# Performance work log

Measured on AMD Instinct MI355X. Metric: run time of the kernel, lower is better.

Reference implementation:

```python
import math
import jax, jax.numpy as jnp
import numpy as np

B, T, E = 2, 2048, 2048
H, HKV = 16, 4
DH = E // H              # 128
ROT_DIM = DH             # rotary_pct = 1.0 -> 128
ROT_HALF = ROT_DIM // 2  # RotaryEmbedding is built with dim=ROT_DIM//2=64; only these dims rotate
MAX_SEQ = 2048


def _rope_tables():
    # theta = 10000 ** (-arange(0, dim, 2)/dim) with dim = ROT_HALF
    theta = 10000.0 ** (-jnp.arange(0, ROT_HALF, 2, dtype=jnp.float32) / ROT_HALF)  # [ROT_HALF//2]
    pos = jnp.arange(MAX_SEQ, dtype=jnp.float32)
    angles = pos[:, None] * theta[None, :]   # [MAX_SEQ, ROT_HALF//2]
    return jnp.cos(angles), jnp.sin(angles)


def _apply_rotary(q, k, start_pos):
    # q: [B,T,H,ROT_DIM], k: [B,T,HKV,ROT_DIM]; rotate only first ROT_HALF dims (interleaved pairs)
    cos, sin = _rope_tables()
    t = q.shape[1]
    cos = jax.lax.dynamic_slice_in_dim(cos, start_pos, t, axis=0)[None, :, None, :]
    sin = jax.lax.dynamic_slice_in_dim(sin, start_pos, t, axis=0)[None, :, None, :]

    def rot(a):
        a_rot, a_pass = a[..., :ROT_HALF], a[..., ROT_HALF:]
        x, y = a_rot[..., 0::2], a_rot[..., 1::2]
        rx = x * cos - y * sin
        ry = x * sin + y * cos
        rotated = jnp.stack([rx, ry], axis=-1).reshape(*a_rot.shape)
        return jnp.concatenate([rotated, a_pass], axis=-1)

    return rot(q), rot(k)


def setup_inputs() -> dict:
    key = jax.random.key(0)
    ks = jax.random.split(key, 9)
    s = 0.02  # weight scale for sane logits
    return {
        "x": jax.random.normal(ks[0], (B, T, E), dtype=jnp.float32),
        "Wq": jax.random.normal(ks[1], (E, H * DH), dtype=jnp.float32) * s,
        "bq": jax.random.normal(ks[2], (H * DH,), dtype=jnp.float32) * s,
        "Wk": jax.random.normal(ks[3], (E, HKV * DH), dtype=jnp.float32) * s,
        "bk": jax.random.normal(ks[4], (HKV * DH,), dtype=jnp.float32) * s,
        "Wv": jax.random.normal(ks[5], (E, HKV * DH), dtype=jnp.float32) * s,
        "bv": jax.random.normal(ks[6], (HKV * DH,), dtype=jnp.float32) * s,
        "Wo": jax.random.normal(ks[7], (E, E), dtype=jnp.float32) * s,
        "bo": jax.random.normal(ks[8], (E,), dtype=jnp.float32) * s,
        "start_pos": 0,
    }


def reference(x, Wq, bq, Wk, bk, Wv, bv, Wo, bo, start_pos):
    b, t, _ = x.shape
    q = (x @ Wq + bq).reshape(b, t, H, DH)
    k = (x @ Wk + bk).reshape(b, t, HKV, DH)
    v = (x @ Wv + bv).reshape(b, t, HKV, DH)

    q, k = _apply_rotary(q, k, start_pos)

    group = H // HKV
    k = jnp.repeat(k, group, axis=2)  # [b,t,H,DH]
    v = jnp.repeat(v, group, axis=2)

    # scores: [b,H,t,t]
    scores = jnp.einsum("bqhd,bkhd->bhqk", q, k) / math.sqrt(DH)
    causal = jnp.tril(jnp.ones((t, t), dtype=bool))
    scores = jnp.where(causal[None, None], scores, -jnp.inf)
    probs = jax.nn.softmax(scores, axis=-1)

    out = jnp.einsum("bhqk,bkhd->bqhd", probs, v).reshape(b, t, H * DH)
    return out @ Wo + bo
```

## Files before the change

### kernel.cpp

```cpp
#include <hip/hip_runtime.h>

typedef __attribute__((ext_vector_type(8))) short short8;
typedef __attribute__((ext_vector_type(4))) float f32x4;
typedef __attribute__((ext_vector_type(16))) float f32x16;

#define DEVFN __device__ __forceinline__

DEVFN unsigned short f2bf(float f) {
  unsigned int u = __builtin_bit_cast(unsigned int, f);
  u += 0x7FFFu + ((u >> 16) & 1u);
  return (unsigned short)(u >> 16);
}
DEVFN float bf2f(unsigned int u) { return __builtin_bit_cast(float, u << 16); }

DEVFN unsigned int cvtpk_bf16(float lo, float hi) {
  unsigned int d;
  asm("v_cvt_pk_bf16_f32 %0, %1, %2" : "=v"(d) : "v"(lo), "v"(hi));
  return d;
}
DEVFN void plswap32(unsigned int& a, unsigned int& b) {
  asm("v_permlane32_swap_b32 %0, %1" : "+v"(a), "+v"(b));
}
DEVFN float bcast32(float v, int srclane) {
  int r = __builtin_amdgcn_ds_bpermute(srclane * 4, __builtin_bit_cast(int, v));
  return __builtin_bit_cast(float, r);
}

__global__ __launch_bounds__(256) void prep_all(
    const float* __restrict__ Wq, const float* __restrict__ Wk, const float* __restrict__ Wv,
    const float* __restrict__ Wo, const float* __restrict__ bq, const float* __restrict__ bk,
    const float* __restrict__ bv, const float* __restrict__ x,
    unsigned short* __restrict__ Wqkvt, unsigned short* __restrict__ Wot,
    unsigned short* __restrict__ xb, float* __restrict__ cost, float* __restrict__ sint,
    float* __restrict__ bcat) {
  __shared__ float lds[32][33];
  const int bid = blockIdx.x, tid = threadIdx.x;
  if (bid < 10240) {
    const float* W; unsigned short* Wt; int ncols, bx, by;
    if (bid < 4096)      { W = Wq; Wt = Wqkvt;                        ncols = 2048; bx = bid & 63; by = bid >> 6; }
    else if (bid < 5120) { int l = bid - 4096; W = Wk; Wt = Wqkvt + (size_t)2048 * 2048; ncols = 512; bx = l & 15; by = l >> 4; }
    else if (bid < 6144) { int l = bid - 5120; W = Wv; Wt = Wqkvt + (size_t)2560 * 2048; ncols = 512; bx = l & 15; by = l >> 4; }
    else                 { int l = bid - 6144; W = Wo; Wt = Wot;      ncols = 2048; bx = l & 63; by = l >> 6; }
    int n0 = bx * 32, k0 = by * 32;
    int tx = tid & 31, ty = tid >> 5;
    #pragma unroll
    for (int i = 0; i < 4; i++) {
      int kr = ty + i * 8;
      lds[kr][tx] = W[(size_t)(k0 + kr) * ncols + n0 + tx];
    }
    __syncthreads();
    #pragma unroll
    for (int i = 0; i < 4; i++) {
      int nr = ty + i * 8;
      Wt[(size_t)(n0 + nr) * 2048 + k0 + tx] = f2bf(lds[tx][nr]);
    }
  } else if (bid < 14336) {
    int gid = (bid - 10240) * 256 + tid;
    const float4* xv = (const float4*)x;
    float4 a = xv[(size_t)gid * 2], b = xv[(size_t)gid * 2 + 1];
    short8 u;
    u[0] = (short)f2bf(a.x); u[1] = (short)f2bf(a.y); u[2] = (short)f2bf(a.z); u[3] = (short)f2bf(a.w);
    u[4] = (short)f2bf(b.x); u[5] = (short)f2bf(b.y); u[6] = (short)f2bf(b.z); u[7] = (short)f2bf(b.w);
    *(short8*)(xb + (size_t)gid * 8) = u;
  } else if (bid < 14592) {
    int gid = (bid - 14336) * 256 + tid;
    int pos = gid >> 5, i = gid & 31;
    float theta = powf(10000.0f, -(float)(2 * i) / 64.0f);
    float ang = (float)pos * theta;
    cost[gid] = cosf(ang);
    sint[gid] = sinf(ang);
  } else {
    int i = (bid - 14592) * 256 + tid;
    float v;
    if (i < 2048) v = bq[i];
    else if (i < 2560) v = bk[i - 2048];
    else v = bv[i - 2560];
    bcat[i] = v;
  }
}

__global__ __launch_bounds__(256) void scatter_all(
    const unsigned short* __restrict__ QKVb, const float* __restrict__ cost,
    const float* __restrict__ sint, const int* __restrict__ spp,
    unsigned short* __restrict__ QFr, unsigned short* __restrict__ KFr,
    unsigned short* __restrict__ VFr) {
  __shared__ __align__(16) unsigned short lds[64 * 128];
  const int bid = blockIdx.x, tid = threadIdx.x;
  if (bid < 20480) {
    int NH, LOG2NH, colOff, gid;
    unsigned short* dst;
    float scale;
    if (bid < 16384) { NH = 16; LOG2NH = 4; colOff = 0;    dst = QFr; scale = 0.12751743f; gid = bid * 256 + tid; }
    else             { NH = 4;  LOG2NH = 2; colOff = 2048; dst = KFr; scale = 1.0f;        gid = (bid - 16384) * 256 + tid; }
    int j = gid & 63;
    int h = (gid >> 6) & (NH - 1);
    int m = gid >> (6 + LOG2NH);
    int t = m & 2047;
    int b = m >> 11;
    const unsigned short* src = QKVb + (size_t)m * 3072 + colOff + h * 128 + 2 * j;
    unsigned int pair = *(const unsigned int*)src;
    float xv = bf2f(pair & 0xFFFFu), yv = bf2f(pair >> 16);
    float rx, ry;
    if (j < 32) {
      int pos = (spp[0] + t) & 2047;
      float c = cost[pos * 32 + j], s = sint[pos * 32 + j];
      rx = xv * c - yv * s;
      ry = xv * s + yv * c;
    } else { rx = xv; ry = yv; }
    rx *= scale; ry *= scale;
    int d0 = 2 * j;
    size_t off = (size_t)(b * NH + h) * 262144 + (t >> 5) * 4096 + (d0 >> 4) * 512
               + ((d0 >> 3) & 1) * 256 + (t & 31) * 8 + (d0 & 7);
    unsigned int outp = (unsigned int)f2bf(rx) | ((unsigned int)f2bf(ry) << 16);
    *(unsigned int*)(dst + off) = outp;
  } else {
    int l = bid - 20480;
    int t0 = (l & 31) * 64;
    int bk = l >> 5;
    const unsigned short* src = QKVb + (size_t)(bk >> 2) * 2048 * 3072 + 2560 + (bk & 3) * 128;
    #pragma unroll
    for (int c = 0; c < 4; c++) {
      int idx = c * 256 + tid;
      int tr = idx >> 4, dc = idx & 15;
      short8 v = *(const short8*)(src + (size_t)(t0 + tr) * 3072 + dc * 8);
      *(short8*)((char*)lds + tr * 256 + 16 * (dc ^ (tr >> 3))) = v;
    }
    __syncthreads();
    unsigned short* dstb = VFr + (size_t)bk * 262144;
    #pragma unroll
    for (int c2 = 0; c2 < 4; c2++) {
      int idx2 = c2 * 256 + tid;
      int tc = idx2 & 7, d = idx2 >> 3;
      short8 u;
      #pragma unroll
      for (int e = 0; e < 8; e++) {
        int t = 8 * tc + e;
        u[e] = *(const short*)((char*)lds + t * 256 + 16 * ((d >> 3) ^ tc) + (d & 7) * 2);
      }
      size_t off = (size_t)(t0 >> 6) * 8192 + ((d >> 5) * 4 + ((tc >> 1) & 3)) * 512
                 + (tc & 1) * 256 + (d & 31) * 8;
      *(short8*)(dstb + off) = u;
    }
  }
}

template<bool BF16OUT>
__global__ __launch_bounds__(256, 2) void gemm_bt(
    const unsigned short* __restrict__ A, const unsigned short* __restrict__ Bt,
    const float* __restrict__ bias, void* __restrict__ Cout, int M, int N, int K, int NTX) {
  __shared__ __align__(16) unsigned short Asl[128 * 64];
  __shared__ __align__(16) unsigned short Bsl[128 * 64];
  int tid = threadIdx.x;
  int lane = tid & 63, w = tid >> 6;
  int wr = w >> 1, wc = w & 1;
  int f = blockIdx.x;
  int cpx = gridDim.x >> 3;
  int fs = (f & 7) * cpx + (f >> 3);
  int m0 = (fs / NTX) * 128, n0 = (fs % NTX) * 128;

  f32x4 acc[4][4];
  #pragma unroll
  for (int i = 0; i < 4; i++)
    #pragma unroll
    for (int j = 0; j < 4; j++)
      #pragma unroll
      for (int r = 0; r < 4; r++) acc[i][j][r] = 0.f;

  int srow = w * 32 + (lane >> 3);
  int kc8 = (lane & 7) * 8;
  const unsigned short* Aptr = A + (size_t)(m0 + srow) * K + kc8;
  const unsigned short* Bptr = Bt + (size_t)(n0 + srow) * K + kc8;
  unsigned short* AslW = Asl + w * 4 * 512;
  unsigned short* BslW = Bsl + w * 4 * 512;

  for (int k0 = 0; k0 < K; k0 += 64) {
    __syncthreads();
    #pragma unroll
    for (int i = 0; i < 4; i++) {
      __builtin_amdgcn_global_load_lds(
        (const __attribute__((address_space(1))) unsigned int*)(Aptr + (size_t)i * 8 * K + k0),
        (__attribute__((address_space(3))) unsigned int*)(AslW + i * 512), 16, 0, 0);
      __builtin_amdgcn_global_load_lds(
        (const __attribute__((address_space(1))) unsigned int*)(Bptr + (size_t)i * 8 * K + k0),
        (__attribute__((address_space(3))) unsigned int*)(BslW + i * 512), 16, 0, 0);
    }
    __syncthreads();
    #pragma unroll
    for (int ks = 0; ks < 2; ks++) {
      short8 af[4], bfr[4];
      #pragma unroll
      for (int mi = 0; mi < 4; mi++)
        af[mi] = *(const short8*)(Asl + (wr * 64 + mi * 16 + (lane & 15)) * 64 + ks * 32 + (lane >> 4) * 8);
      #pragma unroll
      for (int ni = 0; ni < 4; ni++)
        bfr[ni] = *(const short8*)(Bsl + (wc * 64 + ni * 16 + (lane & 15)) * 64 + ks * 32 + (lane >> 4) * 8);
      #pragma unroll
      for (int mi = 0; mi < 4; mi++)
        #pragma unroll
        for (int ni = 0; ni < 4; ni++)
          acc[mi][ni] = __builtin_amdgcn_mfma_f32_16x16x32_bf16(af[mi], bfr[ni], acc[mi][ni], 0, 0, 0);
    }
  }
  int cl = lane & 15, rq = lane >> 4;
  #pragma unroll
  for (int mi = 0; mi < 4; mi++) {
    #pragma unroll
    for (int ni = 0; ni < 4; ni++) {
      int gn = n0 + wc * 64 + ni * 16 + cl;
      float bv = bias[gn];
      #pragma unroll
      for (int r = 0; r < 4; r++) {
        int gm = m0 + wr * 64 + mi * 16 + rq * 4 + r;
        float v = acc[mi][ni][r] + bv;
        if (BF16OUT) ((unsigned short*)Cout)[(size_t)gm * N + gn] = f2bf(v);
        else ((float*)Cout)[(size_t)gm * N + gn] = v;
      }
    }
  }
}

__global__ __launch_bounds__(512, 1) void attn_kernel(
    const unsigned short* __restrict__ QF, const unsigned short* __restrict__ KF,
    const unsigned short* __restrict__ VF, unsigned short* __restrict__ O) {
  const int tid = threadIdx.x;
  const int lane = tid & 63;
  const int w = tid >> 6;
  const int l31 = lane & 31;
  const int hf = lane >> 5;
  const int g = blockIdx.x & 7, j = blockIdx.x >> 3;
  const int b = g >> 2, kh = g & 3;
  const int h = kh * 4 + (j & 3);
  const int i4 = (j >> 2) * 4;
  const int qt = (w < 4) ? (i4 + w) : (67 - i4 - w);
  const int qw = qt * 32;
  const int nt = (qt >> 1) + 1;

  const unsigned short* qh  = QF + (size_t)(b * 16 + h) * 262144 + qt * 4096;
  const unsigned short* khp = KF + (size_t)(b * 4 + kh) * 262144;
  const unsigned short* vhp = VF + (size_t)(b * 4 + kh) * 262144;

  short8 qf[8];
  #pragma unroll
  for (int s = 0; s < 8; s++)
    qf[s] = *(const short8*)(qh + s * 512 + lane * 8);

  short8 ones;
  #pragma unroll
  for (int e = 0; e < 8; e++) ones[e] = (short)0x3F80;

  float m_r = -3.0e38f;
  f32x16 oacc[4];
  f32x16 lacc;
  #pragma unroll
  for (int dt = 0; dt < 4; dt++)
    #pragma unroll
    for (int r = 0; r < 16; r++) oacc[dt][r] = 0.f;
  #pragma unroll
  for (int r = 0; r < 16; r++) lacc[r] = 0.f;

  for (int kt = 0; kt < nt; kt++) {
    const int kv0 = kt * 64;
    f32x16 sc[2];
    {
      short8 kf0[8];
      #pragma unroll
      for (int s = 0; s < 8; s++)
        kf0[s] = *(const short8*)(khp + (size_t)(2 * kt) * 4096 + s * 512 + lane * 8);
      #pragma unroll
      for (int r = 0; r < 16; r++) sc[0][r] = 0.f;
      #pragma unroll
      for (int s = 0; s < 8; s++)
        sc[0] = __builtin_amdgcn_mfma_f32_32x32x16_bf16(kf0[s], qf[s], sc[0], 0, 0, 0);
    }
    {
      short8 kf1[8];
      #pragma unroll
      for (int s = 0; s < 8; s++)
        kf1[s] = *(const short8*)(khp + (size_t)(2 * kt + 1) * 4096 + s * 512 + lane * 8);
      #pragma unroll
      for (int r = 0; r < 16; r++) sc[1][r] = 0.f;
      #pragma unroll
      for (int s = 0; s < 8; s++)
        sc[1] = __builtin_amdgcn_mfma_f32_32x32x16_bf16(kf1[s], qf[s], sc[1], 0, 0, 0);
    }
    short8 vf[4][4];
    #pragma unroll
    for (int dt = 0; dt < 4; dt++)
      #pragma unroll
      for (int ks = 0; ks < 4; ks++)
        vf[dt][ks] = *(const short8*)(vhp + (size_t)kt * 8192 + (dt * 4 + ks) * 512 + lane * 8);

    if (kv0 + 63 > qw) {
      #pragma unroll
      for (int ct = 0; ct < 2; ct++)
        #pragma unroll
        for (int r = 0; r < 16; r++) {
          int kg = kv0 + ct * 32 + (r & 3) + 8 * (r >> 2) + 4 * hf;
          if (kg > qw + l31) sc[ct][r] = -3.0e38f;
        }
    }
    float mx[16];
    #pragma unroll
    for (int r = 0; r < 16; r++) mx[r] = fmaxf(sc[0][r], sc[1][r]);
    #pragma unroll
    for (int s2 = 8; s2 >= 1; s2 >>= 1)
      #pragma unroll
      for (int i = 0; i < 8; i++) if (i < s2) mx[i] = fmaxf(mx[i], mx[i + s2]);
    float tm = fmaxf(mx[0], __shfl_xor(mx[0], 32));
    if (__any(tm > m_r + 8.0f)) {
      float mn = fmaxf(m_r, tm);
      float al = __builtin_amdgcn_exp2f(m_r - mn);
      m_r = mn;
      #pragma unroll
      for (int r = 0; r < 16; r++) {
        float alr = bcast32(al, (r & 3) + 8 * (r >> 2) + 4 * hf);
        #pragma unroll
        for (int dt = 0; dt < 4; dt++) oacc[dt][r] *= alr;
        lacc[r] *= alr;
      }
    }
    #pragma unroll
    for (int ct = 0; ct < 2; ct++)
      #pragma unroll
      for (int r = 0; r < 16; r++) sc[ct][r] = __builtin_amdgcn_exp2f(sc[ct][r] - m_r);

    short8 pa[4];
    #pragma unroll
    for (int ks = 0; ks < 4; ks++) {
      const int ct = ks >> 1, kb = (ks & 1) * 8;
      unsigned int A0 = cvtpk_bf16(sc[ct][kb + 0], sc[ct][kb + 1]);
      unsigned int A1 = cvtpk_bf16(sc[ct][kb + 2], sc[ct][kb + 3]);
      unsigned int B0 = cvtpk_bf16(sc[ct][kb + 4], sc[ct][kb + 5]);
      unsigned int B1 = cvtpk_bf16(sc[ct][kb + 6], sc[ct][kb + 7]);
      plswap32(A0, B0);
      plswap32(A1, B1);
      union { unsigned int wds[4]; short8 s8; } u;
      u.wds[0] = A0; u.wds[1] = A1; u.wds[2] = B0; u.wds[3] = B1;
      pa[ks] = u.s8;
    }
    #pragma unroll
    for (int ks = 0; ks < 4; ks++)
      lacc = __builtin_amdgcn_mfma_f32_32x32x16_bf16(pa[ks], ones, lacc, 0, 0, 0);
    #pragma unroll
    for (int dt = 0; dt < 4; dt++)
      #pragma unroll
      for (int ks = 0; ks < 4; ks++)
        oacc[dt] = __builtin_amdgcn_mfma_f32_32x32x16_bf16(pa[ks], vf[dt][ks], oacc[dt], 0, 0, 0);
  }
  #pragma unroll
  for (int r = 0; r < 16; r++) {
    float inv = 1.0f / lacc[r];
    int rloc = (r & 3) + 8 * (r >> 2) + 4 * hf;
    int qgr = qw + rloc;
    unsigned short* orow = O + ((size_t)(b * 2048 + qgr)) * 2048 + h * 128;
    #pragma unroll
    for (int dt = 0; dt < 4; dt++)
      orow[dt * 32 + l31] = f2bf(oacc[dt][r] * inv);
  }
}

extern "C" void kernel_launch(void* const* d_in, const int* in_sizes, int n_in,
                              void* d_out, int out_size, void* d_ws, size_t ws_size,
                              hipStream_t stream) {
  (void)in_sizes; (void)n_in; (void)out_size; (void)ws_size;
  const float* x  = (const float*)d_in[0];
  const float* Wq = (const float*)d_in[1];
  const float* bq = (const float*)d_in[2];
  const float* Wk = (const float*)d_in[3];
  const float* bk = (const float*)d_in[4];
  const float* Wv = (const float*)d_in[5];
  const float* bv = (const float*)d_in[6];
  const float* Wo = (const float*)d_in[7];
  const float* bo = (const float*)d_in[8];
  const int*   sp = (const int*)d_in[9];

  char* ws = (char*)d_ws;
  unsigned short* xb    = (unsigned short*)ws;
  unsigned short* Wqkvt = (unsigned short*)(ws + 16777216);
  unsigned short* Wot   = (unsigned short*)(ws + 29360128);
  unsigned short* QKVb  = (unsigned short*)(ws + 37748736);
  float* cost           = (float*)(ws + 62914560);
  float* sint           = (float*)(ws + 63176704);
  float* bcat           = (float*)(ws + 63438848);

  unsigned short* Obuf = xb;
  unsigned short* QFr = (unsigned short*)d_out;
  unsigned short* KFr = (unsigned short*)((char*)d_out + 16777216);
  unsigned short* VFr = (unsigned short*)((char*)d_out + 20971520);

  prep_all<<<dim3(14604), 256, 0, stream>>>(Wq, Wk, Wv, Wo, bq, bk, bv, x,
                                            Wqkvt, Wot, xb, cost, sint, bcat);
  gemm_bt<true><<<dim3(768), 256, 0, stream>>>(xb, Wqkvt, bcat, QKVb, 4096, 3072, 2048, 24);
  scatter_all<<<dim3(20736), 256, 0, stream>>>(QKVb, cost, sint, sp, QFr, KFr, VFr);
  attn_kernel<<<dim3(256), 512, 0, stream>>>(QFr, KFr, VFr, Obuf);
  gemm_bt<false><<<dim3(512), 256, 0, stream>>>(Obuf, Wot, bo, (float*)d_out, 4096, 2048, 2048, 16);
}
```

Baseline: 219.0 us.

## Stage K/V tiles in LDS with double-buffered async loads, 4-wave blocks

The attention kernel now stages each 64-key K and V tile into shared memory using global_load_lds, double-buffered so the next tile loads while the current one is consumed. All four waves in a block, which hold adjacent query tiles, share each staged tile instead of each wave reading K/V from global memory directly. Blocks shrink from 512 to 256 threads and the grid doubles, with heavy and light query groups interleaved across the grid for load balance. The cost is a __syncthreads per key tile, plus idle waves in blocks whose query tiles need fewer key tiles than the block's longest wave.

Measured after the change: 218.5 us. No clear change (-0.3%).

```diff
diff --git a/kernel.cpp b/kernel.cpp
--- a/kernel.cpp
+++ b/kernel.cpp
@@ -219,21 +219,26 @@
   }
 }
 
-__global__ __launch_bounds__(512, 1) void attn_kernel(
+__global__ __launch_bounds__(256, 2) void attn_kernel(
     const unsigned short* __restrict__ QF, const unsigned short* __restrict__ KF,
     const unsigned short* __restrict__ VF, unsigned short* __restrict__ O) {
+  __shared__ __align__(16) unsigned short Kl[2][8192];
+  __shared__ __align__(16) unsigned short Vl[2][8192];
+
   const int tid = threadIdx.x;
   const int lane = tid & 63;
   const int w = tid >> 6;
   const int l31 = lane & 31;
   const int hf = lane >> 5;
-  const int g = blockIdx.x & 7, j = blockIdx.x >> 3;
-  const int b = g >> 2, kh = g & 3;
-  const int h = kh * 4 + (j & 3);
-  const int i4 = (j >> 2) * 4;
-  const int qt = (w < 4) ? (i4 + w) : (67 - i4 - w);
+  const int bid = blockIdx.x;
+  const int g8 = bid & 7;
+  const int b = g8 >> 2, kh = g8 & 3;
+  const int h = kh * 4 + ((bid >> 3) & 3);
+  const int qg = (bid < 256) ? (bid >> 5) : (15 - ((bid - 256) >> 5));
+  const int qt = qg * 4 + w;
   const int qw = qt * 32;
-  const int nt = (qt >> 1) + 1;
+  const int ntw = (qt >> 1) + 1;
+  const int nbt = 2 * qg + 2;
 
   const unsigned short* qh  = QF + (size_t)(b * 16 + h) * 262144 + qt * 4096;
   const unsigned short* khp = KF + (size_t)(b * 4 + kh) * 262144;
@@ -258,94 +263,116 @@
   #pragma unroll
   for (int r = 0; r < 16; r++) lacc[r] = 0.f;
 
-  for (int kt = 0; kt < nt; kt++) {
-    const int kv0 = kt * 64;
-    f32x16 sc[2];
-    {
-      short8 kf0[8];
-      #pragma unroll
-      for (int s = 0; s < 8; s++)
-        kf0[s] = *(const short8*)(khp + (size_t)(2 * kt) * 4096 + s * 512 + lane * 8);
-      #pragma unroll
-      for (int r = 0; r < 16; r++) sc[0][r] = 0.f;
-      #pragma unroll
-      for (int s = 0; s < 8; s++)
-        sc[0] = __builtin_amdgcn_mfma_f32_32x32x16_bf16(kf0[s], qf[s], sc[0], 0, 0, 0);
-    }
-    {
-      short8 kf1[8];
-      #pragma unroll
-      for (int s = 0; s < 8; s++)
-        kf1[s] = *(const short8*)(khp + (size_t)(2 * kt + 1) * 4096 + s * 512 + lane * 8);
-      #pragma unroll
-      for (int r = 0; r < 16; r++) sc[1][r] = 0.f;
-      #pragma unroll
-      for (int s = 0; s < 8; s++)
-        sc[1] = __builtin_amdgcn_mfma_f32_32x32x16_bf16(kf1[s], qf[s], sc[1], 0, 0, 0);
-    }
-    short8 vf[4][4];
-    #pragma unroll
-    for (int dt = 0; dt < 4; dt++)
+  auto STAGE = [&](int buf, int kt) {
+    #pragma unroll
+    for (int c = 0; c < 4; c++) {
+      const int sl = w * 4 + c;
+      __builtin_amdgcn_global_load_lds(
+        (const __attribute__((address_space(1))) unsigned int*)(khp + (size_t)kt * 8192 + sl * 512 + lane * 8),
+        (__attribute__((address_space(3))) unsigned int*)(&Kl[buf][sl * 512]), 16, 0, 0);
+      __builtin_amdgcn_global_load_lds(
+        (const __attribute__((address_space(1))) unsigned int*)(vhp + (size_t)kt * 8192 + sl * 512 + lane * 8),
+        (__attribute__((address_space(3))) unsigned int*)(&Vl[buf][sl * 512]), 16, 0, 0);
+    }
+  };
+
+  STAGE(0, 0);
+  int cur = 0;
+  for (int kt = 0; kt < nbt; kt++) {
+    __syncthreads();
+    if (kt + 1 < nbt) STAGE(cur ^ 1, kt + 1);
+    if (kt < ntw) {
+      const int kv0 = kt * 64;
+      const unsigned short* Kb = &Kl[cur][0];
+      const unsigned short* Vb = &Vl[cur][0];
+      f32x16 sc[2];
+      {
+        short8 kf0[8];
+        #pragma unroll
+        for (int s = 0; s < 8; s++)
+          kf0[s] = *(const short8*)(Kb + s * 512 + lane * 8);
+        #pragma unroll
+        for (int r = 0; r < 16; r++) sc[0][r] = 0.f;
+        #pragma unroll
+        for (int s = 0; s < 8; s++)
+          sc[0] = __builtin_amdgcn_mfma_f32_32x32x16_bf16(kf0[s], qf[s], sc[0], 0, 0, 0);
+      }
+      {
+        short8 kf1[8];
+        #pragma unroll
+        for (int s = 0; s < 8; s++)
+          kf1[s] = *(const short8*)(Kb + (8 + s) * 512 + lane * 8);
+        #pragma unroll
+        for (int r = 0; r < 16; r++) sc[1][r] = 0.f;
+        #pragma unroll
+        for (int s = 0; s < 8; s++)
+          sc[1] = __builtin_amdgcn_mfma_f32_32x32x16_bf16(kf1[s], qf[s], sc[1], 0, 0, 0);
+      }
+      short8 vf[4][4];
+      #pragma unroll
+      for (int dt = 0; dt < 4; dt++)
+        #pragma unroll
+        for (int ks = 0; ks < 4; ks++)
+          vf[dt][ks] = *(const short8*)(Vb + (dt * 4 + ks) * 512 + lane * 8);
+
+      if (kv0 + 63 > qw) {
+        #pragma unroll
+        for (int ct = 0; ct < 2; ct++)
+          #pragma unroll
+          for (int r = 0; r < 16; r++) {
+            int kg = kv0 + ct * 32 + (r & 3) + 8 * (r >> 2) + 4 * hf;
+            if (kg > qw + l31) sc[ct][r] = -3.0e38f;
+          }
+      }
+      float mx[16];
+      #pragma unroll
+      for (int r = 0; r < 16; r++) mx[r] = fmaxf(sc[0][r], sc[1][r]);
+      #pragma unroll
+      for (int s2 = 8; s2 >= 1; s2 >>= 1)
+        #pragma unroll
+        for (int i = 0; i < 8; i++) if (i < s2) mx[i] = fmaxf(mx[i], mx[i + s2]);
+      float tm = fmaxf(mx[0], __shfl_xor(mx[0], 32));
+      if (__any(tm > m_r + 8.0f)) {
+        float mn = fmaxf(m_r, tm);
+        float al = __builtin_amdgcn_exp2f(m_r - mn);
+        m_r = mn;
+        #pragma unroll
+        for (int r = 0; r < 16; r++) {
+          float alr = bcast32(al, (r & 3) + 8 * (r >> 2) + 4 * hf);
+          #pragma unroll
+          for (int dt = 0; dt < 4; dt++) oacc[dt][r] *= alr;
+          lacc[r] *= alr;
+        }
+      }
+      #pragma unroll
+      for (int ct = 0; ct < 2; ct++)
+        #pragma unroll
+        for (int r = 0; r < 16; r++) sc[ct][r] = __builtin_amdgcn_exp2f(sc[ct][r] - m_r);
+
+      short8 pa[4];
+      #pragma unroll
+      for (int ks = 0; ks < 4; ks++) {
+        const int ct = ks >> 1, kb = (ks & 1) * 8;
+        unsigned int A0 = cvtpk_bf16(sc[ct][kb + 0], sc[ct][kb + 1]);
+        unsigned int A1 = cvtpk_bf16(sc[ct][kb + 2], sc[ct][kb + 3]);
+        unsigned int B0 = cvtpk_bf16(sc[ct][kb + 4], sc[ct][kb + 5]);
+        unsigned int B1 = cvtpk_bf16(sc[ct][kb + 6], sc[ct][kb + 7]);
+        plswap32(A0, B0);
+        plswap32(A1, B1);
+        union { unsigned int wds[4]; short8 s8; } u;
+        u.wds[0] = A0; u.wds[1] = A1; u.wds[2] = B0; u.wds[3] = B1;
+        pa[ks] = u.s8;
+      }
       #pragma unroll
       for (int ks = 0; ks < 4; ks++)
-        vf[dt][ks] = *(const short8*)(vhp + (size_t)kt * 8192 + (dt * 4 + ks) * 512 + lane * 8);
-
-    if (kv0 + 63 > qw) {
-      #pragma unroll
-      for (int ct = 0; ct < 2; ct++)
-        #pragma unroll
-        for (int r = 0; r < 16; r++) {
-          int kg = kv0 + ct * 32 + (r & 3) + 8 * (r >> 2) + 4 * hf;
-          if (kg > qw + l31) sc[ct][r] = -3.0e38f;
-        }
-    }
-    float mx[16];
-    #pragma unroll
-    for (int r = 0; r < 16; r++) mx[r] = fmaxf(sc[0][r], sc[1][r]);
-    #pragma unroll
-    for (int s2 = 8; s2 >= 1; s2 >>= 1)
-      #pragma unroll
-      for (int i = 0; i < 8; i++) if (i < s2) mx[i] = fmaxf(mx[i], mx[i + s2]);
-    float tm = fmaxf(mx[0], __shfl_xor(mx[0], 32));
-    if (__any(tm > m_r + 8.0f)) {
-      float mn = fmaxf(m_r, tm);
-      float al = __builtin_amdgcn_exp2f(m_r - mn);
-      m_r = mn;
-      #pragma unroll
-      for (int r = 0; r < 16; r++) {
-        float alr = bcast32(al, (r & 3) + 8 * (r >> 2) + 4 * hf);
-        #pragma unroll
-        for (int dt = 0; dt < 4; dt++) oacc[dt][r] *= alr;
-        lacc[r] *= alr;
-      }
-    }
-    #pragma unroll
-    for (int ct = 0; ct < 2; ct++)
-      #pragma unroll
-      for (int r = 0; r < 16; r++) sc[ct][r] = __builtin_amdgcn_exp2f(sc[ct][r] - m_r);
-
-    short8 pa[4];
-    #pragma unroll
-    for (int ks = 0; ks < 4; ks++) {
-      const int ct = ks >> 1, kb = (ks & 1) * 8;
-      unsigned int A0 = cvtpk_bf16(sc[ct][kb + 0], sc[ct][kb + 1]);
-      unsigned int A1 = cvtpk_bf16(sc[ct][kb + 2], sc[ct][kb + 3]);
-      unsigned int B0 = cvtpk_bf16(sc[ct][kb + 4], sc[ct][kb + 5]);
-      unsigned int B1 = cvtpk_bf16(sc[ct][kb + 6], sc[ct][kb + 7]);
-      plswap32(A0, B0);
-      plswap32(A1, B1);
-      union { unsigned int wds[4]; short8 s8; } u;
-      u.wds[0] = A0; u.wds[1] = A1; u.wds[2] = B0; u.wds[3] = B1;
-      pa[ks] = u.s8;
-    }
-    #pragma unroll
-    for (int ks = 0; ks < 4; ks++)
-      lacc = __builtin_amdgcn_mfma_f32_32x32x16_bf16(pa[ks], ones, lacc, 0, 0, 0);
-    #pragma unroll
-    for (int dt = 0; dt < 4; dt++)
-      #pragma unroll
-      for (int ks = 0; ks < 4; ks++)
-        oacc[dt] = __builtin_amdgcn_mfma_f32_32x32x16_bf16(pa[ks], vf[dt][ks], oacc[dt], 0, 0, 0);
+        lacc = __builtin_amdgcn_mfma_f32_32x32x16_bf16(pa[ks], ones, lacc, 0, 0, 0);
+      #pragma unroll
+      for (int dt = 0; dt < 4; dt++)
+        #pragma unroll
+        for (int ks = 0; ks < 4; ks++)
+          oacc[dt] = __builtin_amdgcn_mfma_f32_32x32x16_bf16(pa[ks], vf[dt][ks], oacc[dt], 0, 0, 0);
+    }
+    cur ^= 1;
   }
   #pragma unroll
   for (int r = 0; r < 16; r++) {
@@ -392,6 +419,6 @@
                                             Wqkvt, Wot, xb, cost, sint, bcat);
   gemm_bt<true><<<dim3(768), 256, 0, stream>>>(xb, Wqkvt, bcat, QKVb, 4096, 3072, 2048, 24);
   scatter_all<<<dim3(20736), 256, 0, stream>>>(QKVb, cost, sint, sp, QFr, KFr, VFr);
-  attn_kernel<<<dim3(256), 512, 0, stream>>>(QFr, KFr, VFr, Obuf);
+  attn_kernel<<<dim3(512), 256, 0, stream>>>(QFr, KFr, VFr, Obuf);
   gemm_bt<false><<<dim3(512), 256, 0, stream>>>(Obuf, Wot, bo, (float*)d_out, 4096, 2048, 2048, 16);
 }
```
